# Kernel tuning notes

Hardware: AMD Instinct MI355X
Metric: run time of the kernel (lower is better)

The kernel has to match this reference:

```python
import jax, jax.numpy as jnp
import numpy as np

TOPK = 3
RAT_S = 0.05


def _zero_window_mask(h, w, rat_s=RAT_S):
    # mask[src_pixel, tgt_r, tgt_c] = 1 - gauss_r * gauss_c, gaussian centered at src pixel
    sr = h * rat_s
    sc = w * rat_s
    rows = jnp.arange(h, dtype=jnp.float32)
    cols = jnp.arange(w, dtype=jnp.float32)
    gr = jnp.exp(-((rows[None, :] - rows[:, None]) ** 2) / (2.0 * sr * sr))  # (h_src, h_tgt)
    gc = jnp.exp(-((cols[None, :] - cols[:, None]) ** 2) / (2.0 * sc * sc))  # (w_src, w_tgt)
    mask = 1.0 - gr[:, None, :, None] * gc[None, :, None, :]                 # (h,w,h,w)
    return mask.reshape(h * w, h * w)


def setup_inputs() -> dict:
    key = jax.random.key(0)
    b, c, h, w = 2, 256, 64, 64
    x = jax.random.normal(key, (b, c, h, w), dtype=jnp.float32)
    alpha = jnp.float32(5.0)
    return {"x": x, "alpha": alpha}


def reference(x, alpha):
    b, c, h, w = x.shape
    hw = h * w
    # L2-normalize over channels (F.normalize eps=1e-12 uses max(norm, eps))
    nrm = jnp.sqrt(jnp.sum(x * x, axis=1, keepdims=True))
    xn = x / jnp.maximum(nrm, 1e-12)
    xf = xn.reshape(b, c, hw)
    # (b, hw_src, hw_tgt) affinity
    aff = jnp.einsum('bcs,bct->bst', xf, xf)
    mask = _zero_window_mask(h, w)
    x_aff = aff * mask[None]                               # (b, hw, hw)
    logits = x_aff * alpha
    x_c = jax.nn.softmax(logits, axis=-1) * jax.nn.softmax(logits, axis=-2)
    xc_o = x_c.reshape(b, hw, h, w)
    # top-k over source-pixel axis (dim=-3)
    val = jax.lax.top_k(jnp.moveaxis(xc_o, 1, -1), TOPK)[0]  # (b,h,w,k)
    val = jnp.moveaxis(val, -1, 1)                           # (b,k,h,w)
    x_soft = xc_o / (jnp.sum(xc_o, axis=1, keepdims=True) + 1e-8)
    return (val, x_soft)
```

## Files before the change

### kernel.cpp

```cpp
#include <hip/hip_runtime.h>

#define HW 4096
#define CDIM 256
#define BK 32

typedef _Float16 half8 __attribute__((ext_vector_type(8)));
typedef float f32x4 __attribute__((ext_vector_type(4)));

__device__ __forceinline__ void top3_ins(float v, float& a0, float& a1, float& a2) {
  float m01 = fminf(a0, v);
  a0 = fmaxf(a0, v);
  float m12 = fminf(a1, m01);
  a1 = fmaxf(a1, m01);
  a2 = fmaxf(a2, m12);
}

__device__ __forceinline__ float mask_val(const float* gtab, int s, int t) {
  int dr = (s >> 6) - (t >> 6); dr = dr < 0 ? -dr : dr;
  int dc = (s & 63) - (t & 63); dc = dc < 0 ? -dc : dc;
  return 1.0f - gtab[dr] * gtab[dc];
}

__device__ __forceinline__ void async_copy16(const void* g, void* l) {
  __builtin_amdgcn_global_load_lds((const __attribute__((address_space(1))) void*)g,
                                   (__attribute__((address_space(3))) void*)l, 16, 0, 0);
}

__device__ __forceinline__ void stage_slice(const _Float16* __restrict__ X,
                                            int rowBase, int k0,
                                            _Float16* sdst, int w, int lane) {
  const int csrc = ((lane & 3) - ((lane >> 3) & 3)) & 3;
#pragma unroll
  for (int i = 0; i < 2; ++i) {
    const int rchunk = w * 32 + i * 16;
    const _Float16* g =
        X + (size_t)(rowBase + rchunk + (lane >> 2)) * CDIM + k0 + csrc * 8;
    async_copy16(g, sdst + rchunk * BK);
  }
}

__global__ void __launch_bounds__(256) normalize_k(const float* __restrict__ x,
                                                   _Float16* __restrict__ Xf) {
  const int p = threadIdx.x & 31;
  const int g = threadIdx.x >> 5;
  const int P0 = blockIdx.x * 32;
  const int b = P0 >> 12;
  const int ph = (P0 & (HW - 1)) + p;
  const float* xb = x + (size_t)b * CDIM * HW + ph;
  float vals[32];
  float ss = 0.f;
#pragma unroll
  for (int k = 0; k < 32; ++k) {
    float v = xb[(size_t)(g * 32 + k) * HW];
    vals[k] = v;
    ss += v * v;
  }
  __shared__ float ssqp[8][33];
  __shared__ float scl[32];
  ssqp[g][p] = ss;
  __syncthreads();
  if (threadIdx.x < 32) {
    float s2 = 0.f;
#pragma unroll
    for (int gg = 0; gg < 8; ++gg) s2 += ssqp[gg][threadIdx.x];
    scl[threadIdx.x] = 1.0f / fmaxf(sqrtf(s2), 1e-12f);
  }
  __syncthreads();
  const float sc = scl[p];
  _Float16* o = Xf + (size_t)(P0 + p) * CDIM + g * 32;
#pragma unroll
  for (int c8 = 0; c8 < 4; ++c8) {
    half8 h;
#pragma unroll
    for (int j = 0; j < 8; ++j) h[j] = (_Float16)(vals[c8 * 8 + j] * sc);
    *(half8*)(o + c8 * 8) = h;
  }
}

__global__ void __launch_bounds__(256, 3) gemmE_k(const _Float16* __restrict__ Xf,
                                                  const float* __restrict__ alphap,
                                                  float* __restrict__ R,
                                                  float* __restrict__ Q) {
  __shared__ _Float16 sA[2][128 * BK];
  __shared__ _Float16 sB[2][128 * BK];
  __shared__ float gtab[64];
  if (threadIdx.x < 64) {
    float d = (float)threadIdx.x;
    gtab[threadIdx.x] = __expf(-d * d * 0.048828125f);
  }
  const float alpha = alphap[0];
  const int b = blockIdx.z;
  const _Float16* X = Xf + (size_t)b * HW * CDIM;
  const int lane = threadIdx.x & 63;
  const int w = threadIdx.x >> 6;
  const int wr = w >> 1, wc = w & 1;
  const int mBase = blockIdx.y * 128;
  const int nBase = blockIdx.x * 128;

  f32x4 acc[4][4];
#pragma unroll
  for (int mi = 0; mi < 4; ++mi)
#pragma unroll
    for (int ni = 0; ni < 4; ++ni) acc[mi][ni] = (f32x4){0.f, 0.f, 0.f, 0.f};

  const int aRow0 = wr * 64 + (lane & 15);
  const int bRow0 = wc * 64 + (lane & 15);
  const int cswz = (((lane >> 4) + ((lane >> 1) & 3)) & 3) * 8;

  stage_slice(X, mBase, 0, sA[0], w, lane);
  stage_slice(X, nBase, 0, sB[0], w, lane);

  int cur = 0;
#pragma unroll
  for (int k0 = 0; k0 < CDIM; k0 += BK) {
    __syncthreads();
    if (k0 + BK < CDIM) {
      stage_slice(X, mBase, k0 + BK, sA[cur ^ 1], w, lane);
      stage_slice(X, nBase, k0 + BK, sB[cur ^ 1], w, lane);
    }
    half8 a[4], bfr[4];
#pragma unroll
    for (int i = 0; i < 4; ++i)
      a[i] = *(const half8*)(sA[cur] + (aRow0 + 16 * i) * BK + cswz);
#pragma unroll
    for (int i = 0; i < 4; ++i)
      bfr[i] = *(const half8*)(sB[cur] + (bRow0 + 16 * i) * BK + cswz);
#pragma unroll
    for (int mi = 0; mi < 4; ++mi)
#pragma unroll
      for (int ni = 0; ni < 4; ++ni)
        acc[mi][ni] = __builtin_amdgcn_mfma_f32_16x16x32_f16(a[mi], bfr[ni], acc[mi][ni], 0, 0, 0);
    cur ^= 1;
  }

  const int quad = lane >> 4;
  float* Qb = Q + (size_t)b * HW * HW;
  float csum[4] = {0.f, 0.f, 0.f, 0.f};
#pragma unroll
  for (int mi = 0; mi < 4; ++mi) {
#pragma unroll
    for (int r = 0; r < 4; ++r) {
      const int s = mBase + wr * 64 + mi * 16 + quad * 4 + r;
      float* orow = Qb + (size_t)s * HW;
#pragma unroll
      for (int ni = 0; ni < 4; ++ni) {
        const int t = nBase + wc * 64 + ni * 16 + (lane & 15);
        float e = __expf(alpha * mask_val(gtab, s, t) * acc[mi][ni][r]);
        csum[ni] += e;
        orow[t] = e * e;
      }
    }
  }
#pragma unroll
  for (int off = 16; off < 64; off <<= 1)
#pragma unroll
    for (int ni = 0; ni < 4; ++ni) csum[ni] += __shfl_xor(csum[ni], off);
  if (quad == 0) {
#pragma unroll
    for (int ni = 0; ni < 4; ++ni)
      atomicAdd(&R[b * HW + nBase + wc * 64 + ni * 16 + (lane & 15)], csum[ni]);
  }
}

__global__ void __launch_bounds__(256) colstats_k(const float* __restrict__ Q,
                                                  const float* __restrict__ R,
                                                  float* __restrict__ T,
                                                  float* __restrict__ part) {
  const int b = blockIdx.z;
  const float* Qb = Q + (size_t)b * HW * HW;
  const float* Rb = R + b * HW;
  const int s0 = blockIdx.x * 1024;
  const int t0 = blockIdx.y * 64;
  const int tg = threadIdx.x & 15;
  const int sr = threadIdx.x >> 4;
  float ts[4] = {0.f, 0.f, 0.f, 0.f};
  float q0[4] = {0.f, 0.f, 0.f, 0.f}, q1[4] = {0.f, 0.f, 0.f, 0.f}, q2[4] = {0.f, 0.f, 0.f, 0.f};
#pragma unroll 4
  for (int k = 0; k < 64; ++k) {
    const int s = s0 + k * 16 + sr;
    const float inv = 1.0f / Rb[s];
    f32x4 ev = *(const f32x4*)(Qb + (size_t)s * HW + t0 + tg * 4);
#pragma unroll
    for (int j = 0; j < 4; ++j) {
      float gval = ev[j] * inv;
      ts[j] += gval;
      top3_ins(gval, q0[j], q1[j], q2[j]);
    }
  }
  __shared__ float Tp[16][68], P0a[16][68], P1a[16][68], P2a[16][68];
#pragma unroll
  for (int j = 0; j < 4; ++j) {
    Tp[sr][tg * 4 + j] = ts[j];
    P0a[sr][tg * 4 + j] = q0[j];
    P1a[sr][tg * 4 + j] = q1[j];
    P2a[sr][tg * 4 + j] = q2[j];
  }
  __syncthreads();
  if (threadIdx.x < 64) {
    float tsum = 0.f, a0 = 0.f, a1 = 0.f, a2 = 0.f;
#pragma unroll
    for (int s2 = 0; s2 < 16; ++s2) {
      tsum += Tp[s2][threadIdx.x];
      top3_ins(P0a[s2][threadIdx.x], a0, a1, a2);
      top3_ins(P1a[s2][threadIdx.x], a0, a1, a2);
      top3_ins(P2a[s2][threadIdx.x], a0, a1, a2);
    }
    const int t = t0 + threadIdx.x;
    atomicAdd(&T[b * HW + t], tsum);
    float* pp = part + ((size_t)(b * 4 + blockIdx.x) * HW + t) * 3;
    pp[0] = a0;
    pp[1] = a1;
    pp[2] = a2;
  }
}

__global__ void __launch_bounds__(256) merge_k(const float* __restrict__ R,
                                               const float* __restrict__ T,
                                               const float* __restrict__ part,
                                               float* __restrict__ W,
                                               float* __restrict__ val_out) {
  const int idx = blockIdx.x * 256 + threadIdx.x;
  const int b = idx >> 12;
  const int t = idx & (HW - 1);
  float a0 = 0.f, a1 = 0.f, a2 = 0.f;
#pragma unroll
  for (int c = 0; c < 4; ++c) {
    const float* pp = part + ((size_t)(b * 4 + c) * HW + t) * 3;
    top3_ins(pp[0], a0, a1, a2);
    top3_ins(pp[1], a0, a1, a2);
    top3_ins(pp[2], a0, a1, a2);
  }
  const float r = R[idx];
  const float invr = 1.0f / r;
  val_out[(b * 3 + 0) * HW + t] = a0 * invr;
  val_out[(b * 3 + 1) * HW + t] = a1 * invr;
  val_out[(b * 3 + 2) * HW + t] = a2 * invr;
  W[idx] = 1.0f / (T[idx] + 1e-8f * r);
}

__global__ void __launch_bounds__(256) writeout_k(const float* __restrict__ R,
                                                  const float* __restrict__ W,
                                                  float* __restrict__ X) {
  const int b = blockIdx.y;
  float* Xb = X + (size_t)b * HW * HW;
  const float* Wb = W + b * HW;
  const float* Rb = R + b * HW;
  const int s0 = blockIdx.x * 16;
#pragma unroll 2
  for (int row = 0; row < 16; ++row) {
    const int s = s0 + row;
    const float inv = 1.0f / Rb[s];
    float* rowp = Xb + (size_t)s * HW;
#pragma unroll
    for (int it = 0; it < 4; ++it) {
      const int t = it * 1024 + threadIdx.x * 4;
      f32x4 ev = *(const f32x4*)(rowp + t);
      f32x4 wv = *(const f32x4*)(Wb + t);
      f32x4 o;
#pragma unroll
      for (int j = 0; j < 4; ++j) o[j] = ev[j] * inv * wv[j];
      *(f32x4*)(rowp + t) = o;
    }
  }
}

extern "C" void kernel_launch(void* const* d_in, const int* in_sizes, int n_in,
                              void* d_out, int out_size, void* d_ws, size_t ws_size,
                              hipStream_t stream) {
  const float* x = (const float*)d_in[0];
  const float* alphap = (const float*)d_in[1];
  float* out = (float*)d_out;
  float* out_val = out;
  float* out_x = out + 2 * 3 * HW;
  char* ws = (char*)d_ws;

  _Float16* Xf = (_Float16*)ws;
  float* R = (float*)(ws + (size_t)4194304);
  float* T = R + 2 * HW;
  float* W = T + 2 * HW;
  float* part = W + 2 * HW;

  hipMemsetAsync(R, 0, (size_t)2 * HW * 2 * sizeof(float), stream);

  normalize_k<<<dim3(256), dim3(256), 0, stream>>>(x, Xf);
  gemmE_k<<<dim3(32, 32, 2), dim3(256), 0, stream>>>(Xf, alphap, R, out_x);
  colstats_k<<<dim3(4, 64, 2), dim3(256), 0, stream>>>(out_x, R, T, part);
  merge_k<<<dim3(32), dim3(256), 0, stream>>>(R, T, part, W, out_val);
  writeout_k<<<dim3(256, 2), dim3(256), 0, stream>>>(R, W, out_x);
}
```

Before: 223.7 us.

## Recompute the affinity GEMM three times instead of storing the full matrix

The pipeline no longer materializes the 4096x4096 exp matrix and then reads it back for column stats and writeout. It now runs the cheap fp16 MFMA GEMM three times: once for row sums, once for column sums plus top-3 (fused into the epilogue with per-block partials), and once to write the final normalized output directly. This trades extra GEMM compute for removing roughly two full passes of read-modify-write over the 134MB output. Partial stats are kept in the output buffer as scratch.

```diff
diff --git a/kernel.cpp b/kernel.cpp
--- a/kernel.cpp
+++ b/kernel.cpp
@@ -77,10 +77,51 @@
   }
 }
 
-__global__ void __launch_bounds__(256, 3) gemmE_k(const _Float16* __restrict__ Xf,
+__device__ __forceinline__ void gemm_mainloop(const _Float16* __restrict__ X,
+                                              int mBase, int nBase, int lane, int w,
+                                              _Float16 (*sA)[128 * BK],
+                                              _Float16 (*sB)[128 * BK],
+                                              f32x4 (&acc)[4][4]) {
+  const int wr = w >> 1, wc = w & 1;
+#pragma unroll
+  for (int mi = 0; mi < 4; ++mi)
+#pragma unroll
+    for (int ni = 0; ni < 4; ++ni) acc[mi][ni] = (f32x4){0.f, 0.f, 0.f, 0.f};
+
+  const int aRow0 = wr * 64 + (lane & 15);
+  const int bRow0 = wc * 64 + (lane & 15);
+  const int cswz = (((lane >> 4) + ((lane >> 1) & 3)) & 3) * 8;
+
+  stage_slice(X, mBase, 0, sA[0], w, lane);
+  stage_slice(X, nBase, 0, sB[0], w, lane);
+
+  int cur = 0;
+#pragma unroll
+  for (int k0 = 0; k0 < CDIM; k0 += BK) {
+    __syncthreads();
+    if (k0 + BK < CDIM) {
+      stage_slice(X, mBase, k0 + BK, sA[cur ^ 1], w, lane);
+      stage_slice(X, nBase, k0 + BK, sB[cur ^ 1], w, lane);
+    }
+    half8 a[4], bfr[4];
+#pragma unroll
+    for (int i = 0; i < 4; ++i)
+      a[i] = *(const half8*)(sA[cur] + (aRow0 + 16 * i) * BK + cswz);
+#pragma unroll
+    for (int i = 0; i < 4; ++i)
+      bfr[i] = *(const half8*)(sB[cur] + (bRow0 + 16 * i) * BK + cswz);
+#pragma unroll
+    for (int mi = 0; mi < 4; ++mi)
+#pragma unroll
+      for (int ni = 0; ni < 4; ++ni)
+        acc[mi][ni] = __builtin_amdgcn_mfma_f32_16x16x32_f16(a[mi], bfr[ni], acc[mi][ni], 0, 0, 0);
+    cur ^= 1;
+  }
+}
+
+__global__ void __launch_bounds__(256, 3) gemmR_k(const _Float16* __restrict__ Xf,
                                                   const float* __restrict__ alphap,
-                                                  float* __restrict__ R,
-                                                  float* __restrict__ Q) {
+                                                  float* __restrict__ R) {
   __shared__ _Float16 sA[2][128 * BK];
   __shared__ _Float16 sB[2][128 * BK];
   __shared__ float gtab[64];
@@ -98,168 +139,188 @@
   const int nBase = blockIdx.x * 128;
 
   f32x4 acc[4][4];
-#pragma unroll
-  for (int mi = 0; mi < 4; ++mi)
-#pragma unroll
-    for (int ni = 0; ni < 4; ++ni) acc[mi][ni] = (f32x4){0.f, 0.f, 0.f, 0.f};
-
-  const int aRow0 = wr * 64 + (lane & 15);
-  const int bRow0 = wc * 64 + (lane & 15);
-  const int cswz = (((lane >> 4) + ((lane >> 1) & 3)) & 3) * 8;
-
-  stage_slice(X, mBase, 0, sA[0], w, lane);
-  stage_slice(X, nBase, 0, sB[0], w, lane);
-
-  int cur = 0;
-#pragma unroll
-  for (int k0 = 0; k0 < CDIM; k0 += BK) {
-    __syncthreads();
-    if (k0 + BK < CDIM) {
-      stage_slice(X, mBase, k0 + BK, sA[cur ^ 1], w, lane);
-      stage_slice(X, nBase, k0 + BK, sB[cur ^ 1], w, lane);
-    }
-    half8 a[4], bfr[4];
-#pragma unroll
-    for (int i = 0; i < 4; ++i)
-      a[i] = *(const half8*)(sA[cur] + (aRow0 + 16 * i) * BK + cswz);
-#pragma unroll
-    for (int i = 0; i < 4; ++i)
-      bfr[i] = *(const half8*)(sB[cur] + (bRow0 + 16 * i) * BK + cswz);
-#pragma unroll
-    for (int mi = 0; mi < 4; ++mi)
-#pragma unroll
-      for (int ni = 0; ni < 4; ++ni)
-        acc[mi][ni] = __builtin_amdgcn_mfma_f32_16x16x32_f16(a[mi], bfr[ni], acc[mi][ni], 0, 0, 0);
-    cur ^= 1;
-  }
+  gemm_mainloop(X, mBase, nBase, lane, w, sA, sB, acc);
 
   const int quad = lane >> 4;
-  float* Qb = Q + (size_t)b * HW * HW;
   float csum[4] = {0.f, 0.f, 0.f, 0.f};
 #pragma unroll
   for (int mi = 0; mi < 4; ++mi) {
 #pragma unroll
     for (int r = 0; r < 4; ++r) {
       const int s = mBase + wr * 64 + mi * 16 + quad * 4 + r;
-      float* orow = Qb + (size_t)s * HW;
+#pragma unroll
+      for (int ni = 0; ni < 4; ++ni) {
+        const int t = nBase + wc * 64 + ni * 16 + (lane & 15);
+        csum[ni] += __expf(alpha * mask_val(gtab, s, t) * acc[mi][ni][r]);
+      }
+    }
+  }
+#pragma unroll
+  for (int off = 16; off < 64; off <<= 1)
+#pragma unroll
+    for (int ni = 0; ni < 4; ++ni) csum[ni] += __shfl_xor(csum[ni], off);
+  if (quad == 0) {
+#pragma unroll
+    for (int ni = 0; ni < 4; ++ni)
+      atomicAdd(&R[b * HW + nBase + wc * 64 + ni * 16 + (lane & 15)], csum[ni]);
+  }
+}
+
+__global__ void __launch_bounds__(256, 3) gemmT_k(const _Float16* __restrict__ Xf,
+                                                  const float* __restrict__ alphap,
+                                                  const float* __restrict__ R,
+                                                  float* __restrict__ part) {
+  __shared__ _Float16 sA[2][128 * BK];
+  __shared__ _Float16 sB[2][128 * BK];
+  __shared__ float gtab[64];
+  __shared__ float sRinv[128];
+  __shared__ float sStats[2][128][4];
+  const int b = blockIdx.z;
+  const int mBase = blockIdx.y * 128;
+  const int nBase = blockIdx.x * 128;
+  if (threadIdx.x < 64) {
+    float d = (float)threadIdx.x;
+    gtab[threadIdx.x] = __expf(-d * d * 0.048828125f);
+  }
+  if (threadIdx.x < 128)
+    sRinv[threadIdx.x] = 1.0f / R[b * HW + mBase + threadIdx.x];
+  const float alpha = alphap[0];
+  const _Float16* X = Xf + (size_t)b * HW * CDIM;
+  const int lane = threadIdx.x & 63;
+  const int w = threadIdx.x >> 6;
+  const int wr = w >> 1, wc = w & 1;
+
+  f32x4 acc[4][4];
+  gemm_mainloop(X, mBase, nBase, lane, w, sA, sB, acc);
+
+  const int quad = lane >> 4;
+  float tsum[4] = {0.f, 0.f, 0.f, 0.f};
+  float q0[4] = {0.f, 0.f, 0.f, 0.f}, q1[4] = {0.f, 0.f, 0.f, 0.f}, q2[4] = {0.f, 0.f, 0.f, 0.f};
+#pragma unroll
+  for (int mi = 0; mi < 4; ++mi) {
+#pragma unroll
+    for (int r = 0; r < 4; ++r) {
+      const int lrow = wr * 64 + mi * 16 + quad * 4 + r;
+      const int s = mBase + lrow;
+      const float inv = sRinv[lrow];
 #pragma unroll
       for (int ni = 0; ni < 4; ++ni) {
         const int t = nBase + wc * 64 + ni * 16 + (lane & 15);
         float e = __expf(alpha * mask_val(gtab, s, t) * acc[mi][ni][r]);
-        csum[ni] += e;
-        orow[t] = e * e;
+        float g = e * e * inv;
+        tsum[ni] += g;
+        top3_ins(g, q0[ni], q1[ni], q2[ni]);
       }
     }
   }
 #pragma unroll
-  for (int off = 16; off < 64; off <<= 1)
-#pragma unroll
-    for (int ni = 0; ni < 4; ++ni) csum[ni] += __shfl_xor(csum[ni], off);
+  for (int off = 16; off < 64; off <<= 1) {
+#pragma unroll
+    for (int ni = 0; ni < 4; ++ni) {
+      tsum[ni] += __shfl_xor(tsum[ni], off);
+      float b0 = __shfl_xor(q0[ni], off);
+      float b1 = __shfl_xor(q1[ni], off);
+      float b2 = __shfl_xor(q2[ni], off);
+      top3_ins(b0, q0[ni], q1[ni], q2[ni]);
+      top3_ins(b1, q0[ni], q1[ni], q2[ni]);
+      top3_ins(b2, q0[ni], q1[ni], q2[ni]);
+    }
+  }
   if (quad == 0) {
 #pragma unroll
-    for (int ni = 0; ni < 4; ++ni)
-      atomicAdd(&R[b * HW + nBase + wc * 64 + ni * 16 + (lane & 15)], csum[ni]);
-  }
-}
-
-__global__ void __launch_bounds__(256) colstats_k(const float* __restrict__ Q,
-                                                  const float* __restrict__ R,
-                                                  float* __restrict__ T,
-                                                  float* __restrict__ part) {
-  const int b = blockIdx.z;
-  const float* Qb = Q + (size_t)b * HW * HW;
-  const float* Rb = R + b * HW;
-  const int s0 = blockIdx.x * 1024;
-  const int t0 = blockIdx.y * 64;
-  const int tg = threadIdx.x & 15;
-  const int sr = threadIdx.x >> 4;
-  float ts[4] = {0.f, 0.f, 0.f, 0.f};
-  float q0[4] = {0.f, 0.f, 0.f, 0.f}, q1[4] = {0.f, 0.f, 0.f, 0.f}, q2[4] = {0.f, 0.f, 0.f, 0.f};
-#pragma unroll 4
-  for (int k = 0; k < 64; ++k) {
-    const int s = s0 + k * 16 + sr;
-    const float inv = 1.0f / Rb[s];
-    f32x4 ev = *(const f32x4*)(Qb + (size_t)s * HW + t0 + tg * 4);
-#pragma unroll
-    for (int j = 0; j < 4; ++j) {
-      float gval = ev[j] * inv;
-      ts[j] += gval;
-      top3_ins(gval, q0[j], q1[j], q2[j]);
-    }
-  }
-  __shared__ float Tp[16][68], P0a[16][68], P1a[16][68], P2a[16][68];
-#pragma unroll
-  for (int j = 0; j < 4; ++j) {
-    Tp[sr][tg * 4 + j] = ts[j];
-    P0a[sr][tg * 4 + j] = q0[j];
-    P1a[sr][tg * 4 + j] = q1[j];
-    P2a[sr][tg * 4 + j] = q2[j];
+    for (int ni = 0; ni < 4; ++ni) {
+      const int col = wc * 64 + ni * 16 + (lane & 15);
+      sStats[wr][col][0] = tsum[ni];
+      sStats[wr][col][1] = q0[ni];
+      sStats[wr][col][2] = q1[ni];
+      sStats[wr][col][3] = q2[ni];
+    }
   }
   __syncthreads();
-  if (threadIdx.x < 64) {
-    float tsum = 0.f, a0 = 0.f, a1 = 0.f, a2 = 0.f;
-#pragma unroll
-    for (int s2 = 0; s2 < 16; ++s2) {
-      tsum += Tp[s2][threadIdx.x];
-      top3_ins(P0a[s2][threadIdx.x], a0, a1, a2);
-      top3_ins(P1a[s2][threadIdx.x], a0, a1, a2);
-      top3_ins(P2a[s2][threadIdx.x], a0, a1, a2);
-    }
-    const int t = t0 + threadIdx.x;
-    atomicAdd(&T[b * HW + t], tsum);
-    float* pp = part + ((size_t)(b * 4 + blockIdx.x) * HW + t) * 3;
-    pp[0] = a0;
-    pp[1] = a1;
-    pp[2] = a2;
+  if (threadIdx.x < 128) {
+    float su = sStats[0][threadIdx.x][0] + sStats[1][threadIdx.x][0];
+    float a0 = sStats[0][threadIdx.x][1];
+    float a1 = sStats[0][threadIdx.x][2];
+    float a2 = sStats[0][threadIdx.x][3];
+    top3_ins(sStats[1][threadIdx.x][1], a0, a1, a2);
+    top3_ins(sStats[1][threadIdx.x][2], a0, a1, a2);
+    top3_ins(sStats[1][threadIdx.x][3], a0, a1, a2);
+    f32x4 o = {su, a0, a1, a2};
+    *(f32x4*)(part + ((size_t)(b * 32 + blockIdx.y) * HW + nBase + threadIdx.x) * 4) = o;
   }
 }
 
 __global__ void __launch_bounds__(256) merge_k(const float* __restrict__ R,
-                                               const float* __restrict__ T,
                                                const float* __restrict__ part,
                                                float* __restrict__ W,
                                                float* __restrict__ val_out) {
   const int idx = blockIdx.x * 256 + threadIdx.x;
   const int b = idx >> 12;
   const int t = idx & (HW - 1);
-  float a0 = 0.f, a1 = 0.f, a2 = 0.f;
-#pragma unroll
-  for (int c = 0; c < 4; ++c) {
-    const float* pp = part + ((size_t)(b * 4 + c) * HW + t) * 3;
-    top3_ins(pp[0], a0, a1, a2);
-    top3_ins(pp[1], a0, a1, a2);
-    top3_ins(pp[2], a0, a1, a2);
+  float T = 0.f, a0 = 0.f, a1 = 0.f, a2 = 0.f;
+#pragma unroll 8
+  for (int sblk = 0; sblk < 32; ++sblk) {
+    f32x4 p = *(const f32x4*)(part + ((size_t)(b * 32 + sblk) * HW + t) * 4);
+    T += p[0];
+    top3_ins(p[1], a0, a1, a2);
+    top3_ins(p[2], a0, a1, a2);
+    top3_ins(p[3], a0, a1, a2);
   }
   const float r = R[idx];
   const float invr = 1.0f / r;
   val_out[(b * 3 + 0) * HW + t] = a0 * invr;
   val_out[(b * 3 + 1) * HW + t] = a1 * invr;
   val_out[(b * 3 + 2) * HW + t] = a2 * invr;
-  W[idx] = 1.0f / (T[idx] + 1e-8f * r);
-}
-
-__global__ void __launch_bounds__(256) writeout_k(const float* __restrict__ R,
+  W[idx] = 1.0f / (T + 1e-8f * r);
+}
+
+__global__ void __launch_bounds__(256, 3) gemmW_k(const _Float16* __restrict__ Xf,
+                                                  const float* __restrict__ alphap,
+                                                  const float* __restrict__ R,
                                                   const float* __restrict__ W,
-                                                  float* __restrict__ X) {
-  const int b = blockIdx.y;
-  float* Xb = X + (size_t)b * HW * HW;
-  const float* Wb = W + b * HW;
-  const float* Rb = R + b * HW;
-  const int s0 = blockIdx.x * 16;
-#pragma unroll 2
-  for (int row = 0; row < 16; ++row) {
-    const int s = s0 + row;
-    const float inv = 1.0f / Rb[s];
-    float* rowp = Xb + (size_t)s * HW;
-#pragma unroll
-    for (int it = 0; it < 4; ++it) {
-      const int t = it * 1024 + threadIdx.x * 4;
-      f32x4 ev = *(const f32x4*)(rowp + t);
-      f32x4 wv = *(const f32x4*)(Wb + t);
-      f32x4 o;
-#pragma unroll
-      for (int j = 0; j < 4; ++j) o[j] = ev[j] * inv * wv[j];
-      *(f32x4*)(rowp + t) = o;
+                                                  float* __restrict__ outX) {
+  __shared__ _Float16 sA[2][128 * BK];
+  __shared__ _Float16 sB[2][128 * BK];
+  __shared__ float gtab[64];
+  __shared__ float sRinv[128];
+  __shared__ float sWc[128];
+  const int b = blockIdx.z;
+  const int mBase = blockIdx.y * 128;
+  const int nBase = blockIdx.x * 128;
+  if (threadIdx.x < 64) {
+    float d = (float)threadIdx.x;
+    gtab[threadIdx.x] = __expf(-d * d * 0.048828125f);
+  }
+  if (threadIdx.x < 128) {
+    sRinv[threadIdx.x] = 1.0f / R[b * HW + mBase + threadIdx.x];
+    sWc[threadIdx.x] = W[b * HW + nBase + threadIdx.x];
+  }
+  const float alpha = alphap[0];
+  const _Float16* X = Xf + (size_t)b * HW * CDIM;
+  const int lane = threadIdx.x & 63;
+  const int w = threadIdx.x >> 6;
+  const int wr = w >> 1, wc = w & 1;
+
+  f32x4 acc[4][4];
+  gemm_mainloop(X, mBase, nBase, lane, w, sA, sB, acc);
+
+  const int quad = lane >> 4;
+  float* Xb = outX + (size_t)b * HW * HW;
+#pragma unroll
+  for (int mi = 0; mi < 4; ++mi) {
+#pragma unroll
+    for (int r = 0; r < 4; ++r) {
+      const int lrow = wr * 64 + mi * 16 + quad * 4 + r;
+      const int s = mBase + lrow;
+      const float inv = sRinv[lrow];
+      float* orow = Xb + (size_t)s * HW;
+#pragma unroll
+      for (int ni = 0; ni < 4; ++ni) {
+        const int col = wc * 64 + ni * 16 + (lane & 15);
+        const int t = nBase + col;
+        float e = __expf(alpha * mask_val(gtab, s, t) * acc[mi][ni][r]);
+        orow[t] = e * e * inv * sWc[col];
+      }
     }
   }
 }
@@ -276,15 +337,14 @@
 
   _Float16* Xf = (_Float16*)ws;
   float* R = (float*)(ws + (size_t)4194304);
-  float* T = R + 2 * HW;
-  float* W = T + 2 * HW;
-  float* part = W + 2 * HW;
-
-  hipMemsetAsync(R, 0, (size_t)2 * HW * 2 * sizeof(float), stream);
+  float* W = R + 2 * HW;
+  float* part = out_x;
+
+  hipMemsetAsync(R, 0, (size_t)2 * HW * sizeof(float), stream);
 
   normalize_k<<<dim3(256), dim3(256), 0, stream>>>(x, Xf);
-  gemmE_k<<<dim3(32, 32, 2), dim3(256), 0, stream>>>(Xf, alphap, R, out_x);
-  colstats_k<<<dim3(4, 64, 2), dim3(256), 0, stream>>>(out_x, R, T, part);
-  merge_k<<<dim3(32), dim3(256), 0, stream>>>(R, T, part, W, out_val);
-  writeout_k<<<dim3(256, 2), dim3(256), 0, stream>>>(R, W, out_x);
-}
+  gemmR_k<<<dim3(32, 32, 2), dim3(256), 0, stream>>>(Xf, alphap, R);
+  gemmT_k<<<dim3(32, 32, 2), dim3(256), 0, stream>>>(Xf, alphap, R, part);
+  merge_k<<<dim3(32), dim3(256), 0, stream>>>(R, part, W, out_val);
+  gemmW_k<<<dim3(32, 32, 2), dim3(256), 0, stream>>>(Xf, alphap, R, W, out_x);
+}
```

Result: no change. 224.7 us (+0.4%).

## Store intermediate exp values as fp16 in-place to halve intermediate traffic

Applied to the files above, without the earlier changes.

The GEMM epilogue now writes exp(logit) as fp16 into the first half of each fp32 output row, instead of writing the squared value as fp32. The column-stats pass reads the fp16 values and squares them in fp32. The writeout kernel reads the fp16 row into registers with a one-row prefetch, then overwrites the same row with the final fp32 values. This roughly halves the bytes written and read for the large intermediate, at the cost of fp16 rounding on the exponentials and a delicate in-place read-before-write ordering.

```diff
diff --git a/kernel.cpp b/kernel.cpp
--- a/kernel.cpp
+++ b/kernel.cpp
@@ -5,6 +5,7 @@
 #define BK 32
 
 typedef _Float16 half8 __attribute__((ext_vector_type(8)));
+typedef _Float16 half4v __attribute__((ext_vector_type(4)));
 typedef float f32x4 __attribute__((ext_vector_type(4)));
 
 __device__ __forceinline__ void top3_ins(float v, float& a0, float& a1, float& a2) {
@@ -77,10 +78,10 @@
   }
 }
 
-__global__ void __launch_bounds__(256, 3) gemmE_k(const _Float16* __restrict__ Xf,
-                                                  const float* __restrict__ alphap,
-                                                  float* __restrict__ R,
-                                                  float* __restrict__ Q) {
+__global__ void __launch_bounds__(256, 3) gemmE16_k(const _Float16* __restrict__ Xf,
+                                                    const float* __restrict__ alphap,
+                                                    float* __restrict__ R,
+                                                    float* __restrict__ outX) {
   __shared__ _Float16 sA[2][128 * BK];
   __shared__ _Float16 sB[2][128 * BK];
   __shared__ float gtab[64];
@@ -134,20 +135,20 @@
   }
 
   const int quad = lane >> 4;
-  float* Qb = Q + (size_t)b * HW * HW;
+  _Float16* Hb = (_Float16*)(outX + (size_t)b * HW * HW);
   float csum[4] = {0.f, 0.f, 0.f, 0.f};
 #pragma unroll
   for (int mi = 0; mi < 4; ++mi) {
 #pragma unroll
     for (int r = 0; r < 4; ++r) {
       const int s = mBase + wr * 64 + mi * 16 + quad * 4 + r;
-      float* orow = Qb + (size_t)s * HW;
+      _Float16* hrow = Hb + (size_t)s * (2 * HW);
 #pragma unroll
       for (int ni = 0; ni < 4; ++ni) {
         const int t = nBase + wc * 64 + ni * 16 + (lane & 15);
         float e = __expf(alpha * mask_val(gtab, s, t) * acc[mi][ni][r]);
         csum[ni] += e;
-        orow[t] = e * e;
+        hrow[t] = (_Float16)e;
       }
     }
   }
@@ -162,12 +163,12 @@
   }
 }
 
-__global__ void __launch_bounds__(256) colstats_k(const float* __restrict__ Q,
-                                                  const float* __restrict__ R,
-                                                  float* __restrict__ T,
-                                                  float* __restrict__ part) {
+__global__ void __launch_bounds__(256) colstats16_k(const float* __restrict__ outX,
+                                                    const float* __restrict__ R,
+                                                    float* __restrict__ T,
+                                                    float* __restrict__ part) {
   const int b = blockIdx.z;
-  const float* Qb = Q + (size_t)b * HW * HW;
+  const _Float16* Hb = (const _Float16*)(outX + (size_t)b * HW * HW);
   const float* Rb = R + b * HW;
   const int s0 = blockIdx.x * 1024;
   const int t0 = blockIdx.y * 64;
@@ -179,10 +180,11 @@
   for (int k = 0; k < 64; ++k) {
     const int s = s0 + k * 16 + sr;
     const float inv = 1.0f / Rb[s];
-    f32x4 ev = *(const f32x4*)(Qb + (size_t)s * HW + t0 + tg * 4);
+    half4v ev = *(const half4v*)(Hb + (size_t)s * (2 * HW) + t0 + tg * 4);
 #pragma unroll
     for (int j = 0; j < 4; ++j) {
-      float gval = ev[j] * inv;
+      float e = (float)ev[j];
+      float gval = e * e * inv;
       ts[j] += gval;
       top3_ins(gval, q0[j], q1[j], q2[j]);
     }
@@ -238,27 +240,47 @@
   W[idx] = 1.0f / (T[idx] + 1e-8f * r);
 }
 
-__global__ void __launch_bounds__(256) writeout_k(const float* __restrict__ R,
-                                                  const float* __restrict__ W,
-                                                  float* __restrict__ X) {
+#define WROWS 8
+__global__ void __launch_bounds__(256) writeout16_k(const float* __restrict__ R,
+                                                    const float* __restrict__ W,
+                                                    float* __restrict__ X) {
   const int b = blockIdx.y;
   float* Xb = X + (size_t)b * HW * HW;
+  const _Float16* Hb = (const _Float16*)Xb;
   const float* Wb = W + b * HW;
   const float* Rb = R + b * HW;
-  const int s0 = blockIdx.x * 16;
-#pragma unroll 2
-  for (int row = 0; row < 16; ++row) {
-    const int s = s0 + row;
-    const float inv = 1.0f / Rb[s];
-    float* rowp = Xb + (size_t)s * HW;
+  const int s0 = blockIdx.x * WROWS;
+  f32x4 wv[4];
+#pragma unroll
+  for (int it = 0; it < 4; ++it)
+    wv[it] = *(const f32x4*)(Wb + it * 1024 + threadIdx.x * 4);
+  half4v ehA[4], ehB[4];
+#pragma unroll
+  for (int it = 0; it < 4; ++it)
+    ehA[it] = *(const half4v*)(Hb + (size_t)s0 * (2 * HW) + it * 1024 + threadIdx.x * 4);
+#pragma unroll
+  for (int row = 0; row < WROWS; ++row) {
+    __syncthreads();
+    if (row + 1 < WROWS) {
+      const _Float16* hn = Hb + (size_t)(s0 + row + 1) * (2 * HW);
+#pragma unroll
+      for (int it = 0; it < 4; ++it) {
+        half4v v = *(const half4v*)(hn + it * 1024 + threadIdx.x * 4);
+        if (row & 1) ehA[it] = v; else ehB[it] = v;
+      }
+    }
+    const float inv = 1.0f / Rb[s0 + row];
+    float* rowp = Xb + (size_t)(s0 + row) * HW;
 #pragma unroll
     for (int it = 0; it < 4; ++it) {
       const int t = it * 1024 + threadIdx.x * 4;
-      f32x4 ev = *(const f32x4*)(rowp + t);
-      f32x4 wv = *(const f32x4*)(Wb + t);
+      half4v cur = (row & 1) ? ehB[it] : ehA[it];
       f32x4 o;
 #pragma unroll
-      for (int j = 0; j < 4; ++j) o[j] = ev[j] * inv * wv[j];
+      for (int j = 0; j < 4; ++j) {
+        float e = (float)cur[j];
+        o[j] = e * e * inv * wv[it][j];
+      }
       *(f32x4*)(rowp + t) = o;
     }
   }
@@ -283,8 +305,8 @@
   hipMemsetAsync(R, 0, (size_t)2 * HW * 2 * sizeof(float), stream);
 
   normalize_k<<<dim3(256), dim3(256), 0, stream>>>(x, Xf);
-  gemmE_k<<<dim3(32, 32, 2), dim3(256), 0, stream>>>(Xf, alphap, R, out_x);
-  colstats_k<<<dim3(4, 64, 2), dim3(256), 0, stream>>>(out_x, R, T, part);
+  gemmE16_k<<<dim3(32, 32, 2), dim3(256), 0, stream>>>(Xf, alphap, R, out_x);
+  colstats16_k<<<dim3(4, 64, 2), dim3(256), 0, stream>>>(out_x, R, T, part);
   merge_k<<<dim3(32), dim3(256), 0, stream>>>(R, T, part, W, out_val);
-  writeout_k<<<dim3(256, 2), dim3(256), 0, stream>>>(R, W, out_x);
-}
+  writeout16_k<<<dim3(512, 2), dim3(256), 0, stream>>>(R, W, out_x);
+}
```

Result: faster. 203.8 us (median of 2 runs) (-8.9%).
